# Kernel tuning notes

Hardware: AMD Instinct MI355X
Metric: run time of the kernel (lower is better)

## Reference

```python
import jax, jax.numpy as jnp
import numpy as np

N = 20000   # nodes per node type
D = 128     # hidden_dim
H = 4       # num_heads
L = 2       # num_layers
E = 80000   # edges per relation


def setup_inputs() -> dict:
    key = jax.random.key(0)
    ks = jax.random.split(key, 24)
    w = lambda i, shape: jax.random.normal(ks[i], shape, dtype=jnp.float32) * 0.05
    ei = lambda i: jax.random.randint(ks[i], (2, E), 0, N, dtype=jnp.int32)
    return {
        'x_my': jax.random.normal(ks[0], (N, D), dtype=jnp.float32),
        'x_opp': jax.random.normal(ks[1], (N, D), dtype=jnp.float32),
        'gat_beats_Wl': w(2, (L, D, H * D)),
        'gat_beats_Wr': w(3, (L, D, H * D)),
        'gat_beats_att': w(4, (L, H, D)),
        'gat_beats_b': w(5, (L, D)),
        'gat_rev_Wl': w(6, (L, D, H * D)),
        'gat_rev_Wr': w(7, (L, D, H * D)),
        'gat_rev_att': w(8, (L, H, D)),
        'gat_rev_b': w(9, (L, D)),
        'cg_lose_Wf': w(10, (L, 2 * D, D)),
        'cg_lose_bf': w(11, (L, D)),
        'cg_lose_Ws': w(12, (L, 2 * D, D)),
        'cg_lose_bs': w(13, (L, D)),
        'cg_rev_Wf': w(14, (L, 2 * D, D)),
        'cg_rev_bf': w(15, (L, D)),
        'cg_rev_Ws': w(16, (L, 2 * D, D)),
        'cg_rev_bs': w(17, (L, D)),
        'nw_W': w(18, (L, D, D)),
        'nw_b': w(19, (L, D)),
        'ei_beats': ei(20),
        'ei_loses': ei(21),
        'ei_rev_beats': ei(22),
        'ei_rev_loses': ei(23),
    }


def _segment_softmax(scores, seg, num):
    # scores [E, H]; softmax over edges sharing the same destination node
    m = jax.ops.segment_max(scores, seg, num_segments=num)
    m = jnp.where(jnp.isfinite(m), m, 0.0)  # empty segments -> -inf guard
    e = jnp.exp(scores - m[seg])
    s = jax.ops.segment_sum(e, seg, num_segments=num)
    return e / (s[seg] + 1e-16)


def _gatv2(x_src, x_dst, src, dst, Wl, Wr, att, b, num_dst):
    # PyG GATv2Conv, heads=H, concat=False, add_self_loops=False
    xl = (x_src @ Wl).reshape(x_src.shape[0], H, D)  # [Ns, H, D]
    xr = (x_dst @ Wr).reshape(x_dst.shape[0], H, D)  # [Nd, H, D]
    z = jax.nn.leaky_relu(xl[src] + xr[dst], negative_slope=0.2)  # [E, H, D]
    score = jnp.einsum('ehd,hd->eh', z, att)
    alpha = _segment_softmax(score, dst, num_dst)
    out = jax.ops.segment_sum(xl[src] * alpha[:, :, None], dst, num_segments=num_dst)
    return out.mean(axis=1) + b  # concat=False -> mean over heads, then bias


def _cgconv(x_src, x_dst, src, dst, Wf, bf, Ws, bs, num_dst):
    # PyG CGConv: z = [x_i (dst), x_j (src)], gate * softplus, aggr='add', residual
    z = jnp.concatenate([x_dst[dst], x_src[src]], axis=-1)  # [E, 2D]
    m = jax.nn.sigmoid(z @ Wf + bf) * jax.nn.softplus(z @ Ws + bs)
    return jax.ops.segment_sum(m, dst, num_segments=num_dst) + x_dst


def reference(x_my, x_opp,
              gat_beats_Wl, gat_beats_Wr, gat_beats_att, gat_beats_b,
              gat_rev_Wl, gat_rev_Wr, gat_rev_att, gat_rev_b,
              cg_lose_Wf, cg_lose_bf, cg_lose_Ws, cg_lose_bs,
              cg_rev_Wf, cg_rev_bf, cg_rev_Ws, cg_rev_bs,
              nw_W, nw_b,
              ei_beats, ei_loses, ei_rev_beats, ei_rev_loses):
    for l in range(L):
        # HeteroConv with aggr='sum': sum per-relation outputs per dst node type
        opp_new = (_gatv2(x_my, x_opp, ei_beats[0], ei_beats[1],
                          gat_beats_Wl[l], gat_beats_Wr[l], gat_beats_att[l], gat_beats_b[l],
                          x_opp.shape[0])
                   + _cgconv(x_my, x_opp, ei_loses[0], ei_loses[1],
                             cg_lose_Wf[l], cg_lose_bf[l], cg_lose_Ws[l], cg_lose_bs[l],
                             x_opp.shape[0]))
        my_new = (_cgconv(x_opp, x_my, ei_rev_beats[0], ei_rev_beats[1],
                          cg_rev_Wf[l], cg_rev_bf[l], cg_rev_Ws[l], cg_rev_bs[l],
                          x_my.shape[0])
                  + _gatv2(x_opp, x_my, ei_rev_loses[0], ei_rev_loses[1],
                           gat_rev_Wl[l], gat_rev_Wr[l], gat_rev_att[l], gat_rev_b[l],
                           x_my.shape[0]))
        # shared nodewise Linear applied to every node type
        x_my = my_new @ nw_W[l] + nw_b[l]
        x_opp = opp_new @ nw_W[l] + nw_b[l]
    return x_my, x_opp
```

## Files before the change

### kernel.cpp

```cpp
#include <hip/hip_runtime.h>
#include <hip/hip_bf16.h>
#include <cstddef>

#define NNODE 20000
#define DDIM  128
#define NHEAD 4
#define NEDGE 80000

typedef __attribute__((ext_vector_type(8))) short short8;
typedef __attribute__((ext_vector_type(4))) float f32x4;

__device__ __forceinline__ float bf2f(unsigned short u) {
  union { unsigned u32; float f; } c; c.u32 = ((unsigned)u) << 16; return c.f;
}
__device__ __forceinline__ unsigned short f2bf(float f) {
  union { float f; unsigned u; } c; c.f = f;
  unsigned u = c.u;
  unsigned r = 0x7FFFu + ((u >> 16) & 1u);
  return (unsigned short)((u + r) >> 16);
}

template<typename AT, typename OutT>
__global__ __launch_bounds__(256, 4) void gemm_mfma(
    const AT* __restrict__ A0, const unsigned short* __restrict__ B0, OutT* __restrict__ C0,
    const AT* __restrict__ A1, const unsigned short* __restrict__ B1, OutT* __restrict__ C1,
    int halfY, int M, int N, const float* __restrict__ bias)
{
  __shared__ unsigned short Bs[128 * 128];
  const int nwgx = gridDim.x;
  const int nwg = nwgx * gridDim.y;
  int orig = blockIdx.x + nwgx * blockIdx.y;
  int q8 = nwg >> 3, r8 = nwg & 7;
  int xc = orig & 7, lo = orig >> 3;
  int wg = ((xc < r8) ? xc * (q8 + 1) : r8 * (q8 + 1) + (xc - r8) * q8) + lo;
  int by = wg / nwgx;
  int bx = wg - by * nwgx;
  const AT* A = A0; const unsigned short* Bt = B0; OutT* C = C0;
  if (by >= halfY) { by -= halfY; A = A1; Bt = B1; C = C1; }
  const int bm = by * 128, bn = bx * 128;
  const int t = threadIdx.x;
  char* bsb = (char*)Bs;

  const char* btile = (const char*)(Bt + (size_t)bn * 128);
  #pragma unroll
  for (int i = 0; i < 8; ++i) {
    int fo = i * 4096 + t * 16;
    int r = fo >> 8, boff = fo & 255;
    short8 v = *reinterpret_cast<const short8*>(btile + fo);
    *reinterpret_cast<short8*>(bsb + r * 256 + (boff ^ ((r & 7) << 4))) = v;
  }
  __syncthreads();

  const int w = t >> 6, wr = w >> 1, wc = w & 1;
  const int lane = t & 63, l15 = lane & 15, lg = lane >> 4;
  const int rowl = bm + wr * 64 + l15;

  f32x4 acc[4][4];
  #pragma unroll
  for (int m = 0; m < 4; ++m)
    #pragma unroll
    for (int n = 0; n < 4; ++n) acc[m][n] = (f32x4){0.f, 0.f, 0.f, 0.f};

  #pragma unroll
  for (int kk = 0; kk < 4; ++kk) {
    const int kb = kk * 32 + lg * 8;
    short8 af[4], bfr[4];
    #pragma unroll
    for (int m = 0; m < 4; ++m) {
      if constexpr (sizeof(AT) == 4) {
        const float* ap = (const float*)A + ((size_t)(rowl + m * 16) << 7) + kb;
        float4 v0 = *reinterpret_cast<const float4*>(ap);
        float4 v1 = *reinterpret_cast<const float4*>(ap + 4);
        short8 hv;
        hv[0] = (short)f2bf(v0.x); hv[1] = (short)f2bf(v0.y);
        hv[2] = (short)f2bf(v0.z); hv[3] = (short)f2bf(v0.w);
        hv[4] = (short)f2bf(v1.x); hv[5] = (short)f2bf(v1.y);
        hv[6] = (short)f2bf(v1.z); hv[7] = (short)f2bf(v1.w);
        af[m] = hv;
      } else {
        af[m] = *reinterpret_cast<const short8*>(
            (const unsigned short*)A + ((size_t)(rowl + m * 16) << 7) + kb);
      }
    }
    const int kbyte = kb * 2;
    #pragma unroll
    for (int n = 0; n < 4; ++n) {
      int r = wc * 64 + n * 16 + l15;
      bfr[n] = *reinterpret_cast<const short8*>(bsb + r * 256 + (kbyte ^ ((r & 7) << 4)));
    }
    #pragma unroll
    for (int m = 0; m < 4; ++m)
      #pragma unroll
      for (int n = 0; n < 4; ++n)
        acc[m][n] = __builtin_amdgcn_mfma_f32_16x16x32_bf16(af[m], bfr[n], acc[m][n], 0, 0, 0);
  }

  #pragma unroll
  for (int m = 0; m < 4; ++m) {
    #pragma unroll
    for (int j = 0; j < 4; ++j) {
      int row = bm + wr * 64 + m * 16 + lg * 4 + j;
      if (row >= M) continue;
      #pragma unroll
      for (int n = 0; n < 4; ++n) {
        int col = bn + wc * 64 + n * 16 + l15;
        float v = acc[m][n][j];
        if (bias) v += bias[col];
        if constexpr (sizeof(OutT) == 2) {
          C[(size_t)row * N + col] = (OutT)f2bf(v);
        } else {
          C[(size_t)row * N + col] = v;
        }
      }
    }
  }
}

__global__ __launch_bounds__(256) void pack_gat(
    const float* __restrict__ gbWl, const float* __restrict__ gbWr,
    const float* __restrict__ grWl, const float* __restrict__ grWr,
    unsigned short* __restrict__ out)
{
  int idx = blockIdx.x * 256 + threadIdx.x;
  if (idx >= 2 * 2 * 1024 * 128) return;
  int k = idx & 127;
  int n = (idx >> 7) & 1023;
  int type = (idx >> 17) & 1;
  int l = idx >> 18;
  const float* W; int col;
  if (type == 0) { if (n < 512) { W = gbWl; col = n; } else { W = grWr; col = n - 512; } }
  else           { if (n < 512) { W = gbWr; col = n; } else { W = grWl; col = n - 512; } }
  out[idx] = f2bf(W[(size_t)l * 128 * 512 + (size_t)k * 512 + col]);
}

__global__ __launch_bounds__(256) void pack_cg(
    const float* __restrict__ clWf, const float* __restrict__ clWs,
    const float* __restrict__ crWf, const float* __restrict__ crWs,
    unsigned short* __restrict__ out)
{
  int idx = blockIdx.x * 256 + threadIdx.x;
  if (idx >= 2 * 2 * 512 * 128) return;
  int k = idx & 127;
  int n = (idx >> 7) & 511;
  int type = (idx >> 16) & 1;
  int l = idx >> 17;
  int blk = n >> 7, c = n & 127;
  const float* W; int row;
  if (type == 0) {
    if (blk == 0) { W = clWf; row = 128 + k; }
    else if (blk == 1) { W = clWs; row = 128 + k; }
    else if (blk == 2) { W = crWf; row = k; }
    else { W = crWs; row = k; }
  } else {
    if (blk == 0) { W = clWf; row = k; }
    else if (blk == 1) { W = clWs; row = k; }
    else if (blk == 2) { W = crWf; row = 128 + k; }
    else { W = crWs; row = 128 + k; }
  }
  out[idx] = f2bf(W[(size_t)l * 256 * 128 + (size_t)row * 128 + c]);
}

__global__ __launch_bounds__(256) void pack_nw(
    const float* __restrict__ nwW, unsigned short* __restrict__ out)
{
  int idx = blockIdx.x * 256 + threadIdx.x;
  if (idx >= 2 * 128 * 128) return;
  int k = idx & 127;
  int n = (idx >> 7) & 127;
  int l = idx >> 14;
  out[idx] = f2bf(nwW[(size_t)l * 128 * 128 + (size_t)k * 128 + n]);
}

__global__ __launch_bounds__(256) void f2b_kernel(
    const float* __restrict__ in, unsigned short* __restrict__ out, int n)
{
  int idx = (blockIdx.x * 256 + threadIdx.x) * 8;
  if (idx >= n) return;
  float4 a = *reinterpret_cast<const float4*>(in + idx);
  float4 b = *reinterpret_cast<const float4*>(in + idx + 4);
  short8 o;
  o[0] = (short)f2bf(a.x); o[1] = (short)f2bf(a.y);
  o[2] = (short)f2bf(a.z); o[3] = (short)f2bf(a.w);
  o[4] = (short)f2bf(b.x); o[5] = (short)f2bf(b.y);
  o[6] = (short)f2bf(b.z); o[7] = (short)f2bf(b.w);
  *reinterpret_cast<short8*>(out + idx) = o;
}

__global__ __launch_bounds__(256) void build_buckets(
    const int* __restrict__ e0, const int* __restrict__ e1,
    const int* __restrict__ e2, const int* __restrict__ e3,
    unsigned* __restrict__ cnt, int* __restrict__ bucket)
{
  int idx = blockIdx.x * 256 + threadIdx.x;
  if (idx >= 4 * NEDGE) return;
  int set = idx / NEDGE;
  int e = idx - set * NEDGE;
  const int* ei = (set == 0) ? e0 : (set == 1) ? e1 : (set == 2) ? e2 : e3;
  int s = ei[e], d = ei[NEDGE + e];
  unsigned slot = atomicAdd(&cnt[set * NNODE + d], 1u);
  if (slot < 64u) bucket[((size_t)set * NNODE + d) * 64 + slot] = s;
}

__global__ __launch_bounds__(256) void edge_fused(
    const unsigned short* __restrict__ xlA, const unsigned short* __restrict__ xrA,
    const unsigned short* __restrict__ FsA, const unsigned short* __restrict__ SsA,
    const unsigned short* __restrict__ FdA, const unsigned short* __restrict__ SdA,
    const unsigned short* __restrict__ xresA,
    const int* __restrict__ bgA, const unsigned* __restrict__ cgA,
    const int* __restrict__ bcA, const unsigned* __restrict__ ccA,
    const float* __restrict__ attA, const float* __restrict__ biasA,
    const float* __restrict__ bfA, const float* __restrict__ bsA,
    float* __restrict__ accA,
    const unsigned short* __restrict__ xlB, const unsigned short* __restrict__ xrB,
    const unsigned short* __restrict__ FsB, const unsigned short* __restrict__ SsB,
    const unsigned short* __restrict__ FdB, const unsigned short* __restrict__ SdB,
    const unsigned short* __restrict__ xresB,
    const int* __restrict__ bgB, const unsigned* __restrict__ cgB,
    const int* __restrict__ bcB, const unsigned* __restrict__ ccB,
    const float* __restrict__ attB, const float* __restrict__ biasB,
    const float* __restrict__ bfB, const float* __restrict__ bsB,
    float* __restrict__ accB, int nwb)
{
  int blk = blockIdx.x;
  int second = (blk >= nwb) ? 1 : 0;
  if (second) blk -= nwb;
  int d = blk * 4 + (threadIdx.x >> 6);
  int lane = threadIdx.x & 63;
  int h = lane >> 4, q = lane & 15;

  const unsigned short* xl  = second ? xlB  : xlA;
  const unsigned short* xr  = second ? xrB  : xrA;
  const unsigned short* Fs  = second ? FsB  : FsA;
  const unsigned short* Ss  = second ? SsB  : SsA;
  const unsigned short* Fd  = second ? FdB  : FdA;
  const unsigned short* Sd  = second ? SdB  : SdA;
  const unsigned short* xres = second ? xresB : xresA;
  const int* bg = second ? bgB : bgA;
  const unsigned* cg = second ? cgB : cgA;
  const int* bc = second ? bcB : bcA;
  const unsigned* cc = second ? ccB : ccA;
  const float* att  = second ? attB  : attA;
  const float* bias = second ? biasB : biasA;
  const float* bf_  = second ? bfB   : bfA;
  const float* bs_  = second ? bsB   : bsA;
  float* acc = second ? accB : accA;

  unsigned ng = cg[d]; ng = (ng > 64u) ? 64u : ng;
  short8 xrv = *reinterpret_cast<const short8*>(xr + (size_t)d * 1024 + h * 128 + q * 8);
  float4 at0 = *reinterpret_cast<const float4*>(att + h * 128 + q * 8);
  float4 at1 = *reinterpret_cast<const float4*>(att + h * 128 + q * 8 + 4);
  float xrf[8], atf[8];
  atf[0] = at0.x; atf[1] = at0.y; atf[2] = at0.z; atf[3] = at0.w;
  atf[4] = at1.x; atf[5] = at1.y; atf[6] = at1.z; atf[7] = at1.w;
  #pragma unroll
  for (int j = 0; j < 8; ++j) xrf[j] = bf2f((unsigned short)xrv[j]);

  float uout[8] = {0.f, 0.f, 0.f, 0.f, 0.f, 0.f, 0.f, 0.f};
  float ssum = 0.f;
  const int* bkg = bg + (size_t)d * 64;
  short8 xln = {0,0,0,0,0,0,0,0};
  if (ng > 0) {
    int s0 = bkg[0];
    xln = *reinterpret_cast<const short8*>(xl + (size_t)s0 * 1024 + h * 128 + q * 8);
  }
  for (unsigned i = 0; i < ng; ++i) {
    short8 xlv = xln;
    if (i + 1 < ng) {
      int s2 = bkg[i + 1];
      xln = *reinterpret_cast<const short8*>(xl + (size_t)s2 * 1024 + h * 128 + q * 8);
    }
    float xlf[8];
    #pragma unroll
    for (int j = 0; j < 8; ++j) xlf[j] = bf2f((unsigned short)xlv[j]);
    float sum = 0.f;
    #pragma unroll
    for (int j = 0; j < 8; ++j) {
      float z = xlf[j] + xrf[j];
      z = (z > 0.f) ? z : 0.2f * z;
      sum += atf[j] * z;
    }
    #pragma unroll
    for (int m = 1; m < 16; m <<= 1) sum += __shfl_xor(sum, m);
    float e = __expf(fminf(sum, 80.f));
    ssum += e;
    #pragma unroll
    for (int j = 0; j < 8; ++j) uout[j] += e * xlf[j];
  }
  float scale = __builtin_amdgcn_rcpf(ssum + 1e-16f) * 0.25f;
  #pragma unroll
  for (int j = 0; j < 8; ++j) {
    float v = uout[j] * scale;
    v += __shfl_xor(v, 16);
    v += __shfl_xor(v, 32);
    uout[j] = v;
  }

  unsigned nc = cc[d]; nc = (nc > 64u) ? 64u : nc;
  float fd[8], sd[8], ac[8];
  {
    short8 fdv = *reinterpret_cast<const short8*>(Fd + (size_t)d * 512 + q * 8);
    short8 sdv = *reinterpret_cast<const short8*>(Sd + (size_t)d * 512 + q * 8);
    const float* bfp = bf_ + q * 8;
    const float* bsp = bs_ + q * 8;
    #pragma unroll
    for (int j = 0; j < 8; ++j) {
      fd[j] = bf2f((unsigned short)fdv[j]) + bfp[j];
      sd[j] = bf2f((unsigned short)sdv[j]) + bsp[j];
      ac[j] = 0.f;
    }
  }
  const int* bkc = bc + (size_t)d * 64;
  short8 fsn = {0,0,0,0,0,0,0,0}, ssn = {0,0,0,0,0,0,0,0};
  unsigned i0 = (unsigned)h;
  if (i0 < nc) {
    int s0 = bkc[i0];
    fsn = *reinterpret_cast<const short8*>(Fs + (size_t)s0 * 512 + q * 8);
    ssn = *reinterpret_cast<const short8*>(Ss + (size_t)s0 * 512 + q * 8);
  }
  for (unsigned i = i0; i < nc; i += 4) {
    short8 fsv = fsn, ssv = ssn;
    if (i + 4 < nc) {
      int s2 = bkc[i + 4];
      fsn = *reinterpret_cast<const short8*>(Fs + (size_t)s2 * 512 + q * 8);
      ssn = *reinterpret_cast<const short8*>(Ss + (size_t)s2 * 512 + q * 8);
    }
    #pragma unroll
    for (int j = 0; j < 8; ++j) {
      float g  = fd[j] + bf2f((unsigned short)fsv[j]);
      float tt = sd[j] + bf2f((unsigned short)ssv[j]);
      float gate = __builtin_amdgcn_rcpf(1.f + __expf(-g));
      float sp = fmaxf(tt, 0.f) + __logf(1.f + __expf(-fabsf(tt)));
      ac[j] += gate * sp;
    }
  }
  #pragma unroll
  for (int j = 0; j < 8; ++j) {
    float v = ac[j];
    v += __shfl_xor(v, 16);
    v += __shfl_xor(v, 32);
    ac[j] = v;
  }

  if (h == 0) {
    short8 xs = *reinterpret_cast<const short8*>(xres + (size_t)d * 128 + q * 8);
    const float* bp = bias + q * 8;
    float4 o0, o1;
    o0.x = uout[0] + ac[0] + bf2f((unsigned short)xs[0]) + bp[0];
    o0.y = uout[1] + ac[1] + bf2f((unsigned short)xs[1]) + bp[1];
    o0.z = uout[2] + ac[2] + bf2f((unsigned short)xs[2]) + bp[2];
    o0.w = uout[3] + ac[3] + bf2f((unsigned short)xs[3]) + bp[3];
    o1.x = uout[4] + ac[4] + bf2f((unsigned short)xs[4]) + bp[4];
    o1.y = uout[5] + ac[5] + bf2f((unsigned short)xs[5]) + bp[5];
    o1.z = uout[6] + ac[6] + bf2f((unsigned short)xs[6]) + bp[6];
    o1.w = uout[7] + ac[7] + bf2f((unsigned short)xs[7]) + bp[7];
    *reinterpret_cast<float4*>(acc + (size_t)d * 128 + q * 8) = o0;
    *reinterpret_cast<float4*>(acc + (size_t)d * 128 + q * 8 + 4) = o1;
  }
}


extern "C" void kernel_launch(void* const* d_in, const int* in_sizes, int n_in,
                              void* d_out, int out_size, void* d_ws, size_t ws_size,
                              hipStream_t stream) {
  const float* x_my_in  = (const float*)d_in[0];
  const float* x_opp_in = (const float*)d_in[1];
  const float* gb_Wl  = (const float*)d_in[2];
  const float* gb_Wr  = (const float*)d_in[3];
  const float* gb_att = (const float*)d_in[4];
  const float* gb_b   = (const float*)d_in[5];
  const float* gr_Wl  = (const float*)d_in[6];
  const float* gr_Wr  = (const float*)d_in[7];
  const float* gr_att = (const float*)d_in[8];
  const float* gr_b   = (const float*)d_in[9];
  const float* cl_Wf  = (const float*)d_in[10];
  const float* cl_bf  = (const float*)d_in[11];
  const float* cl_Ws  = (const float*)d_in[12];
  const float* cl_bs  = (const float*)d_in[13];
  const float* cr_Wf  = (const float*)d_in[14];
  const float* cr_bf  = (const float*)d_in[15];
  const float* cr_Ws  = (const float*)d_in[16];
  const float* cr_bs  = (const float*)d_in[17];
  const float* nw_W   = (const float*)d_in[18];
  const float* nw_b   = (const float*)d_in[19];
  const int* ei_beats     = (const int*)d_in[20];
  const int* ei_loses     = (const int*)d_in[21];
  const int* ei_rev_beats = (const int*)d_in[22];
  const int* ei_rev_loses = (const int*)d_in[23];

  float* out = (float*)d_out;

  const size_t ND = (size_t)NNODE * DDIM;
  unsigned short* XAb = (unsigned short*)d_ws;
  float* NM  = (float*)(XAb + 2 * ND);
  float* NO  = NM + ND;
  unsigned short* PJM = (unsigned short*)(NM + 2 * ND);
  unsigned short* PJO = PJM + (size_t)NNODE * 1024;
  unsigned short* PCM = PJO + (size_t)NNODE * 1024;
  unsigned short* PCO = PCM + (size_t)NNODE * 512;
  unsigned* CNT = (unsigned*)(PCO + (size_t)NNODE * 512);
  int* BKT = (int*)(CNT + 4 * NNODE);
  unsigned short* PKG = (unsigned short*)(BKT + (size_t)4 * NNODE * 64);
  unsigned short* PKC = PKG + 2 * 2 * 1024 * 128;
  unsigned short* PKN = PKC + 2 * 2 * 512 * 128;

  const int cvb = (int)(ND / 8 + 255) / 256;
  const int nwb = NNODE / 4;

  hipLaunchKernelGGL(pack_gat, dim3(2 * 2 * 1024 * 128 / 256), dim3(256), 0, stream,
                     gb_Wl, gb_Wr, gr_Wl, gr_Wr, PKG);
  hipLaunchKernelGGL(pack_cg, dim3(2 * 2 * 512 * 128 / 256), dim3(256), 0, stream,
                     cl_Wf, cl_Ws, cr_Wf, cr_Ws, PKC);
  hipLaunchKernelGGL(pack_nw, dim3(2 * 128 * 128 / 256), dim3(256), 0, stream, nw_W, PKN);

  hipLaunchKernelGGL(f2b_kernel, dim3(cvb), dim3(256), 0, stream, x_my_in,  XAb,      (int)ND);
  hipLaunchKernelGGL(f2b_kernel, dim3(cvb), dim3(256), 0, stream, x_opp_in, XAb + ND, (int)ND);

  hipMemsetAsync(CNT, 0, 4 * NNODE * sizeof(unsigned), stream);
  hipLaunchKernelGGL(build_buckets, dim3((4 * NEDGE + 255) / 256), dim3(256), 0, stream,
                     ei_beats, ei_rev_loses, ei_loses, ei_rev_beats, CNT, BKT);

  for (int l = 0; l < 2; ++l) {
    const size_t oA = (size_t)l * NHEAD * DDIM;
    const size_t oB = (size_t)l * DDIM;

    hipLaunchKernelGGL((gemm_mfma<unsigned short, unsigned short>), dim3(8, 314), dim3(256), 0, stream,
                       XAb,      PKG + (size_t)(l * 2 + 0) * 1024 * 128, PJM,
                       XAb + ND, PKG + (size_t)(l * 2 + 1) * 1024 * 128, PJO,
                       157, NNODE, 1024, (const float*)nullptr);

    hipLaunchKernelGGL((gemm_mfma<unsigned short, unsigned short>), dim3(4, 314), dim3(256), 0, stream,
                       XAb,      PKC + (size_t)(l * 2 + 0) * 512 * 128, PCM,
                       XAb + ND, PKC + (size_t)(l * 2 + 1) * 512 * 128, PCO,
                       157, NNODE, 512, (const float*)nullptr);

    hipLaunchKernelGGL(edge_fused, dim3(2 * nwb), dim3(256), 0, stream,
                        PJM, PJO,
                        PCM, PCM + 128, PCO, PCO + 128,
                        XAb + ND,
                       BKT + (size_t)0 * NNODE * 64, CNT + 0 * NNODE,
                       BKT + (size_t)2 * NNODE * 64, CNT + 2 * NNODE,
                       gb_att + oA, gb_b + oB, cl_bf + oB, cl_bs + oB, NO,
                        PJO + 512, PJM + 512,
                        PCO + 256, PCO + 384, PCM + 256, PCM + 384,
                        XAb,
                       BKT + (size_t)1 * NNODE * 64, CNT + 1 * NNODE,
                       BKT + (size_t)3 * NNODE * 64, CNT + 3 * NNODE,
                       gr_att + oA, gr_b + oB, cr_bf + oB, cr_bs + oB, NM,
                       nwb);

    if (l == 0) {
      hipLaunchKernelGGL((gemm_mfma<float, unsigned short>), dim3(1, 313), dim3(256), 0, stream,
                         NM, PKN + (size_t)l * 128 * 128, XAb,
                         NM, PKN + (size_t)l * 128 * 128, XAb,
                         313, 2 * NNODE, 128, nw_b + oB);
    } else {
      hipLaunchKernelGGL((gemm_mfma<float, float>), dim3(1, 313), dim3(256), 0, stream,
                         NM, PKN + (size_t)l * 128 * 128, out,
                         NM, PKN + (size_t)l * 128 * 128, out,
                         313, 2 * NNODE, 128, nw_b + oB);
    }
  }
  (void)in_sizes; (void)n_in; (void)out_size; (void)ws_size;
}
```

Measured before the change: 439.8 us.

## Merge GAT and CGConv projection GEMMs into one wide GEMM and batch gathers

Packs the GAT and CGConv weights into one 1536-column matrix per layer, so a single GEMM per layer produces both projections into an interleaved row-strided buffer. Also merges the weight-pack and float-to-bf16 conversion kernels into single launches. In the edge kernel, the first four GAT source rows and the first two CGConv rows per lane are loaded up front instead of one-ahead prefetching, to raise memory-level parallelism. The cost is a wider stride in the gathered rows, which may spread them across more cache lines, plus higher register pressure.

```diff
diff --git a/kernel.cpp b/kernel.cpp
--- a/kernel.cpp
+++ b/kernel.cpp
@@ -6,6 +6,7 @@
 #define DDIM  128
 #define NHEAD 4
 #define NEDGE 80000
+#define PSTR  1536
 
 typedef __attribute__((ext_vector_type(8))) short short8;
 typedef __attribute__((ext_vector_type(4))) float f32x4;
@@ -116,68 +117,64 @@
   }
 }
 
-__global__ __launch_bounds__(256) void pack_gat(
+__global__ __launch_bounds__(256) void pack_all(
     const float* __restrict__ gbWl, const float* __restrict__ gbWr,
     const float* __restrict__ grWl, const float* __restrict__ grWr,
-    unsigned short* __restrict__ out)
+    const float* __restrict__ clWf, const float* __restrict__ clWs,
+    const float* __restrict__ crWf, const float* __restrict__ crWs,
+    const float* __restrict__ nwW,
+    unsigned short* __restrict__ PKU, unsigned short* __restrict__ PKN)
 {
   int idx = blockIdx.x * 256 + threadIdx.x;
-  if (idx >= 2 * 2 * 1024 * 128) return;
-  int k = idx & 127;
-  int n = (idx >> 7) & 1023;
-  int type = (idx >> 17) & 1;
-  int l = idx >> 18;
-  const float* W; int col;
-  if (type == 0) { if (n < 512) { W = gbWl; col = n; } else { W = grWr; col = n - 512; } }
-  else           { if (n < 512) { W = gbWr; col = n; } else { W = grWl; col = n - 512; } }
-  out[idx] = f2bf(W[(size_t)l * 128 * 512 + (size_t)k * 512 + col]);
-}
-
-__global__ __launch_bounds__(256) void pack_cg(
-    const float* __restrict__ clWf, const float* __restrict__ clWs,
-    const float* __restrict__ crWf, const float* __restrict__ crWs,
-    unsigned short* __restrict__ out)
-{
-  int idx = blockIdx.x * 256 + threadIdx.x;
-  if (idx >= 2 * 2 * 512 * 128) return;
-  int k = idx & 127;
-  int n = (idx >> 7) & 511;
-  int type = (idx >> 16) & 1;
-  int l = idx >> 17;
-  int blk = n >> 7, c = n & 127;
-  const float* W; int row;
-  if (type == 0) {
-    if (blk == 0) { W = clWf; row = 128 + k; }
-    else if (blk == 1) { W = clWs; row = 128 + k; }
-    else if (blk == 2) { W = crWf; row = k; }
-    else { W = crWs; row = k; }
-  } else {
-    if (blk == 0) { W = clWf; row = k; }
-    else if (blk == 1) { W = clWs; row = k; }
-    else if (blk == 2) { W = crWf; row = 128 + k; }
-    else { W = crWs; row = 128 + k; }
-  }
-  out[idx] = f2bf(W[(size_t)l * 256 * 128 + (size_t)row * 128 + c]);
-}
-
-__global__ __launch_bounds__(256) void pack_nw(
-    const float* __restrict__ nwW, unsigned short* __restrict__ out)
-{
-  int idx = blockIdx.x * 256 + threadIdx.x;
-  if (idx >= 2 * 128 * 128) return;
-  int k = idx & 127;
-  int n = (idx >> 7) & 127;
-  int l = idx >> 14;
-  out[idx] = f2bf(nwW[(size_t)l * 128 * 128 + (size_t)k * 128 + n]);
-}
-
-__global__ __launch_bounds__(256) void f2b_kernel(
-    const float* __restrict__ in, unsigned short* __restrict__ out, int n)
+  const int NU = 2 * 2 * PSTR * 128;
+  if (idx < NU) {
+    int k = idx & 127;
+    int r = idx >> 7;
+    int n = r % PSTR;
+    int rt = r / PSTR;
+    int type = rt & 1, l = rt >> 1;
+    float v;
+    if (n < 1024) {
+      const float* W; int col;
+      if (type == 0) { if (n < 512) { W = gbWl; col = n; } else { W = grWr; col = n - 512; } }
+      else           { if (n < 512) { W = gbWr; col = n; } else { W = grWl; col = n - 512; } }
+      v = W[(size_t)l * 128 * 512 + (size_t)k * 512 + col];
+    } else {
+      int nn = n - 1024, blk = nn >> 7, c = nn & 127;
+      const float* W; int row;
+      if (type == 0) {
+        if (blk == 0) { W = clWf; row = 128 + k; }
+        else if (blk == 1) { W = clWs; row = 128 + k; }
+        else if (blk == 2) { W = crWf; row = k; }
+        else { W = crWs; row = k; }
+      } else {
+        if (blk == 0) { W = clWf; row = k; }
+        else if (blk == 1) { W = clWs; row = k; }
+        else if (blk == 2) { W = crWf; row = 128 + k; }
+        else { W = crWs; row = 128 + k; }
+      }
+      v = W[(size_t)l * 256 * 128 + (size_t)row * 128 + c];
+    }
+    PKU[idx] = f2bf(v);
+    return;
+  }
+  int i2 = idx - NU;
+  if (i2 >= 2 * 128 * 128) return;
+  int k = i2 & 127;
+  int n = (i2 >> 7) & 127;
+  int l = i2 >> 14;
+  PKN[i2] = f2bf(nwW[(size_t)l * 128 * 128 + (size_t)k * 128 + n]);
+}
+
+__global__ __launch_bounds__(256) void f2b_all(
+    const float* __restrict__ inA, const float* __restrict__ inB,
+    unsigned short* __restrict__ out, int nhalf)
 {
   int idx = (blockIdx.x * 256 + threadIdx.x) * 8;
-  if (idx >= n) return;
-  float4 a = *reinterpret_cast<const float4*>(in + idx);
-  float4 b = *reinterpret_cast<const float4*>(in + idx + 4);
+  if (idx >= 2 * nhalf) return;
+  const float* src = (idx < nhalf) ? inA + idx : inB + (idx - nhalf);
+  float4 a = *reinterpret_cast<const float4*>(src);
+  float4 b = *reinterpret_cast<const float4*>(src + 4);
   short8 o;
   o[0] = (short)f2bf(a.x); o[1] = (short)f2bf(a.y);
   o[2] = (short)f2bf(a.z); o[3] = (short)f2bf(a.w);
@@ -202,51 +199,49 @@
 }
 
 __global__ __launch_bounds__(256) void edge_fused(
-    const unsigned short* __restrict__ xlA, const unsigned short* __restrict__ xrA,
-    const unsigned short* __restrict__ FsA, const unsigned short* __restrict__ SsA,
-    const unsigned short* __restrict__ FdA, const unsigned short* __restrict__ SdA,
-    const unsigned short* __restrict__ xresA,
-    const int* __restrict__ bgA, const unsigned* __restrict__ cgA,
-    const int* __restrict__ bcA, const unsigned* __restrict__ ccA,
-    const float* __restrict__ attA, const float* __restrict__ biasA,
-    const float* __restrict__ bfA, const float* __restrict__ bsA,
-    float* __restrict__ accA,
-    const unsigned short* __restrict__ xlB, const unsigned short* __restrict__ xrB,
-    const unsigned short* __restrict__ FsB, const unsigned short* __restrict__ SsB,
-    const unsigned short* __restrict__ FdB, const unsigned short* __restrict__ SdB,
-    const unsigned short* __restrict__ xresB,
-    const int* __restrict__ bgB, const unsigned* __restrict__ cgB,
-    const int* __restrict__ bcB, const unsigned* __restrict__ ccB,
-    const float* __restrict__ attB, const float* __restrict__ biasB,
-    const float* __restrict__ bfB, const float* __restrict__ bsB,
-    float* __restrict__ accB, int nwb)
+    const unsigned short* __restrict__ PJM_, const unsigned short* __restrict__ PJO_,
+    const unsigned short* __restrict__ XAb_,
+    const int* __restrict__ BKT_, const unsigned* __restrict__ CNT_,
+    const float* __restrict__ gb_att, const float* __restrict__ gb_b,
+    const float* __restrict__ cl_bf, const float* __restrict__ cl_bs,
+    const float* __restrict__ gr_att, const float* __restrict__ gr_b,
+    const float* __restrict__ cr_bf, const float* __restrict__ cr_bs,
+    float* __restrict__ NM_, float* __restrict__ NO_, int nwb)
 {
   int blk = blockIdx.x;
-  int second = (blk >= nwb) ? 1 : 0;
+  int second = blk >= nwb;
   if (second) blk -= nwb;
   int d = blk * 4 + (threadIdx.x >> 6);
   int lane = threadIdx.x & 63;
   int h = lane >> 4, q = lane & 15;
 
-  const unsigned short* xl  = second ? xlB  : xlA;
-  const unsigned short* xr  = second ? xrB  : xrA;
-  const unsigned short* Fs  = second ? FsB  : FsA;
-  const unsigned short* Ss  = second ? SsB  : SsA;
-  const unsigned short* Fd  = second ? FdB  : FdA;
-  const unsigned short* Sd  = second ? SdB  : SdA;
-  const unsigned short* xres = second ? xresB : xresA;
-  const int* bg = second ? bgB : bgA;
-  const unsigned* cg = second ? cgB : cgA;
-  const int* bc = second ? bcB : bcA;
-  const unsigned* cc = second ? ccB : ccA;
-  const float* att  = second ? attB  : attA;
-  const float* bias = second ? biasB : biasA;
-  const float* bf_  = second ? bfB   : bfA;
-  const float* bs_  = second ? bsB   : bsA;
-  float* acc = second ? accB : accA;
+  const unsigned short *xl, *xr, *Fs, *Ss, *Fd, *Sd, *xres;
+  const int *bg, *bc;
+  const unsigned *cg, *cc;
+  const float *att, *bias, *bf_, *bs_;
+  float* acc;
+  if (!second) {
+    xl = PJM_;        xr = PJO_;
+    Fs = PJM_ + 1024; Ss = PJM_ + 1152;
+    Fd = PJO_ + 1024; Sd = PJO_ + 1152;
+    xres = XAb_ + (size_t)NNODE * DDIM;
+    bg = BKT_;                              cg = CNT_;
+    bc = BKT_ + (size_t)2 * NNODE * 64;     cc = CNT_ + 2 * NNODE;
+    att = gb_att; bias = gb_b; bf_ = cl_bf; bs_ = cl_bs; acc = NO_;
+  } else {
+    xl = PJO_ + 512;  xr = PJM_ + 512;
+    Fs = PJO_ + 1280; Ss = PJO_ + 1408;
+    Fd = PJM_ + 1280; Sd = PJM_ + 1408;
+    xres = XAb_;
+    bg = BKT_ + (size_t)1 * NNODE * 64;     cg = CNT_ + 1 * NNODE;
+    bc = BKT_ + (size_t)3 * NNODE * 64;     cc = CNT_ + 3 * NNODE;
+    att = gr_att; bias = gr_b; bf_ = cr_bf; bs_ = cr_bs; acc = NM_;
+  }
 
   unsigned ng = cg[d]; ng = (ng > 64u) ? 64u : ng;
-  short8 xrv = *reinterpret_cast<const short8*>(xr + (size_t)d * 1024 + h * 128 + q * 8);
+  const int* bkg = bg + (size_t)d * 64;
+  const size_t off = (size_t)h * 128 + q * 8;
+  short8 xrv = *reinterpret_cast<const short8*>(xr + (size_t)d * PSTR + off);
   float4 at0 = *reinterpret_cast<const float4*>(att + h * 128 + q * 8);
   float4 at1 = *reinterpret_cast<const float4*>(att + h * 128 + q * 8 + 4);
   float xrf[8], atf[8];
@@ -257,34 +252,38 @@
 
   float uout[8] = {0.f, 0.f, 0.f, 0.f, 0.f, 0.f, 0.f, 0.f};
   float ssum = 0.f;
-  const int* bkg = bg + (size_t)d * 64;
-  short8 xln = {0,0,0,0,0,0,0,0};
+
+#define GATP(XLV) { \
+    float xlf[8]; \
+    _Pragma("unroll") for (int j = 0; j < 8; ++j) xlf[j] = bf2f((unsigned short)(XLV)[j]); \
+    float sum = 0.f; \
+    _Pragma("unroll") for (int j = 0; j < 8; ++j) { \
+      float z = xlf[j] + xrf[j]; \
+      z = (z > 0.f) ? z : 0.2f * z; \
+      sum += atf[j] * z; } \
+    _Pragma("unroll") for (int m = 1; m < 16; m <<= 1) sum += __shfl_xor(sum, m); \
+    float e = __expf(fminf(sum, 80.f)); \
+    ssum += e; \
+    _Pragma("unroll") for (int j = 0; j < 8; ++j) uout[j] += e * xlf[j]; }
+
   if (ng > 0) {
     int s0 = bkg[0];
-    xln = *reinterpret_cast<const short8*>(xl + (size_t)s0 * 1024 + h * 128 + q * 8);
-  }
-  for (unsigned i = 0; i < ng; ++i) {
-    short8 xlv = xln;
-    if (i + 1 < ng) {
-      int s2 = bkg[i + 1];
-      xln = *reinterpret_cast<const short8*>(xl + (size_t)s2 * 1024 + h * 128 + q * 8);
-    }
-    float xlf[8];
-    #pragma unroll
-    for (int j = 0; j < 8; ++j) xlf[j] = bf2f((unsigned short)xlv[j]);
-    float sum = 0.f;
-    #pragma unroll
-    for (int j = 0; j < 8; ++j) {
-      float z = xlf[j] + xrf[j];
-      z = (z > 0.f) ? z : 0.2f * z;
-      sum += atf[j] * z;
-    }
-    #pragma unroll
-    for (int m = 1; m < 16; m <<= 1) sum += __shfl_xor(sum, m);
-    float e = __expf(fminf(sum, 80.f));
-    ssum += e;
-    #pragma unroll
-    for (int j = 0; j < 8; ++j) uout[j] += e * xlf[j];
+    int s1 = bkg[(ng > 1u) ? 1 : 0];
+    int s2 = bkg[(ng > 2u) ? 2 : 0];
+    int s3 = bkg[(ng > 3u) ? 3 : 0];
+    short8 x0 = *reinterpret_cast<const short8*>(xl + (size_t)s0 * PSTR + off);
+    short8 x1 = *reinterpret_cast<const short8*>(xl + (size_t)s1 * PSTR + off);
+    short8 x2 = *reinterpret_cast<const short8*>(xl + (size_t)s2 * PSTR + off);
+    short8 x3 = *reinterpret_cast<const short8*>(xl + (size_t)s3 * PSTR + off);
+    GATP(x0);
+    if (ng > 1u) GATP(x1);
+    if (ng > 2u) GATP(x2);
+    if (ng > 3u) GATP(x3);
+    for (unsigned i = 4; i < ng; ++i) {
+      int s = bkg[i];
+      short8 xv = *reinterpret_cast<const short8*>(xl + (size_t)s * PSTR + off);
+      GATP(xv);
+    }
   }
   float scale = __builtin_amdgcn_rcpf(ssum + 1e-16f) * 0.25f;
   #pragma unroll
@@ -296,10 +295,12 @@
   }
 
   unsigned nc = cc[d]; nc = (nc > 64u) ? 64u : nc;
+  const int* bkc = bc + (size_t)d * 64;
+  const size_t offc = (size_t)q * 8;
   float fd[8], sd[8], ac[8];
   {
-    short8 fdv = *reinterpret_cast<const short8*>(Fd + (size_t)d * 512 + q * 8);
-    short8 sdv = *reinterpret_cast<const short8*>(Sd + (size_t)d * 512 + q * 8);
+    short8 fdv = *reinterpret_cast<const short8*>(Fd + (size_t)d * PSTR + offc);
+    short8 sdv = *reinterpret_cast<const short8*>(Sd + (size_t)d * PSTR + offc);
     const float* bfp = bf_ + q * 8;
     const float* bsp = bs_ + q * 8;
     #pragma unroll
@@ -309,28 +310,33 @@
       ac[j] = 0.f;
     }
   }
-  const int* bkc = bc + (size_t)d * 64;
-  short8 fsn = {0,0,0,0,0,0,0,0}, ssn = {0,0,0,0,0,0,0,0};
-  unsigned i0 = (unsigned)h;
-  if (i0 < nc) {
-    int s0 = bkc[i0];
-    fsn = *reinterpret_cast<const short8*>(Fs + (size_t)s0 * 512 + q * 8);
-    ssn = *reinterpret_cast<const short8*>(Ss + (size_t)s0 * 512 + q * 8);
-  }
-  for (unsigned i = i0; i < nc; i += 4) {
-    short8 fsv = fsn, ssv = ssn;
-    if (i + 4 < nc) {
-      int s2 = bkc[i + 4];
-      fsn = *reinterpret_cast<const short8*>(Fs + (size_t)s2 * 512 + q * 8);
-      ssn = *reinterpret_cast<const short8*>(Ss + (size_t)s2 * 512 + q * 8);
-    }
-    #pragma unroll
-    for (int j = 0; j < 8; ++j) {
-      float g  = fd[j] + bf2f((unsigned short)fsv[j]);
-      float tt = sd[j] + bf2f((unsigned short)ssv[j]);
-      float gate = __builtin_amdgcn_rcpf(1.f + __expf(-g));
-      float sp = fmaxf(tt, 0.f) + __logf(1.f + __expf(-fabsf(tt)));
-      ac[j] += gate * sp;
+
+#define CGP(FV, SV) { \
+    _Pragma("unroll") for (int j = 0; j < 8; ++j) { \
+      float g  = fd[j] + bf2f((unsigned short)(FV)[j]); \
+      float tt = sd[j] + bf2f((unsigned short)(SV)[j]); \
+      float gate = __builtin_amdgcn_rcpf(1.f + __expf(-g)); \
+      float sp = fmaxf(tt, 0.f) + __logf(1.f + __expf(-fabsf(tt))); \
+      ac[j] += gate * sp; } }
+
+  {
+    unsigned ia = (unsigned)h, ib2 = (unsigned)h + 4u;
+    bool pa = ia < nc, pb = ib2 < nc;
+    int sa = pa ? bkc[ia] : 0;
+    int sb = pb ? bkc[ib2] : 0;
+    short8 fa = {0,0,0,0,0,0,0,0}, sav = {0,0,0,0,0,0,0,0};
+    short8 fb = {0,0,0,0,0,0,0,0}, sbv = {0,0,0,0,0,0,0,0};
+    if (pa) { fa  = *reinterpret_cast<const short8*>(Fs + (size_t)sa * PSTR + offc);
+              sav = *reinterpret_cast<const short8*>(Ss + (size_t)sa * PSTR + offc); }
+    if (pb) { fb  = *reinterpret_cast<const short8*>(Fs + (size_t)sb * PSTR + offc);
+              sbv = *reinterpret_cast<const short8*>(Ss + (size_t)sb * PSTR + offc); }
+    if (pa) CGP(fa, sav);
+    if (pb) CGP(fb, sbv);
+    for (unsigned i = (unsigned)h + 8u; i < nc; i += 4u) {
+      int s = bkc[i];
+      short8 fv = *reinterpret_cast<const short8*>(Fs + (size_t)s * PSTR + offc);
+      short8 sv = *reinterpret_cast<const short8*>(Ss + (size_t)s * PSTR + offc);
+      CGP(fv, sv);
     }
   }
   #pragma unroll
@@ -394,26 +400,20 @@
   float* NM  = (float*)(XAb + 2 * ND);
   float* NO  = NM + ND;
   unsigned short* PJM = (unsigned short*)(NM + 2 * ND);
-  unsigned short* PJO = PJM + (size_t)NNODE * 1024;
-  unsigned short* PCM = PJO + (size_t)NNODE * 1024;
-  unsigned short* PCO = PCM + (size_t)NNODE * 512;
-  unsigned* CNT = (unsigned*)(PCO + (size_t)NNODE * 512);
+  unsigned short* PJO = PJM + (size_t)NNODE * PSTR;
+  unsigned* CNT = (unsigned*)(PJO + (size_t)NNODE * PSTR);
   int* BKT = (int*)(CNT + 4 * NNODE);
-  unsigned short* PKG = (unsigned short*)(BKT + (size_t)4 * NNODE * 64);
-  unsigned short* PKC = PKG + 2 * 2 * 1024 * 128;
-  unsigned short* PKN = PKC + 2 * 2 * 512 * 128;
-
-  const int cvb = (int)(ND / 8 + 255) / 256;
+  unsigned short* PKU = (unsigned short*)(BKT + (size_t)4 * NNODE * 64);
+  unsigned short* PKN = PKU + 2 * 2 * PSTR * 128;
+
   const int nwb = NNODE / 4;
 
-  hipLaunchKernelGGL(pack_gat, dim3(2 * 2 * 1024 * 128 / 256), dim3(256), 0, stream,
-                     gb_Wl, gb_Wr, gr_Wl, gr_Wr, PKG);
-  hipLaunchKernelGGL(pack_cg, dim3(2 * 2 * 512 * 128 / 256), dim3(256), 0, stream,
-                     cl_Wf, cl_Ws, cr_Wf, cr_Ws, PKC);
-  hipLaunchKernelGGL(pack_nw, dim3(2 * 128 * 128 / 256), dim3(256), 0, stream, nw_W, PKN);
-
-  hipLaunchKernelGGL(f2b_kernel, dim3(cvb), dim3(256), 0, stream, x_my_in,  XAb,      (int)ND);
-  hipLaunchKernelGGL(f2b_kernel, dim3(cvb), dim3(256), 0, stream, x_opp_in, XAb + ND, (int)ND);
+  hipLaunchKernelGGL(pack_all, dim3((2 * 2 * PSTR * 128 + 2 * 128 * 128) / 256), dim3(256),
+                     0, stream, gb_Wl, gb_Wr, gr_Wl, gr_Wr,
+                     cl_Wf, cl_Ws, cr_Wf, cr_Ws, nw_W, PKU, PKN);
+
+  hipLaunchKernelGGL(f2b_all, dim3((int)(2 * ND / 8 / 256)), dim3(256), 0, stream,
+                     x_my_in, x_opp_in, XAb, (int)ND);
 
   hipMemsetAsync(CNT, 0, 4 * NNODE * sizeof(unsigned), stream);
   hipLaunchKernelGGL(build_buckets, dim3((4 * NEDGE + 255) / 256), dim3(256), 0, stream,
@@ -423,30 +423,16 @@
     const size_t oA = (size_t)l * NHEAD * DDIM;
     const size_t oB = (size_t)l * DDIM;
 
-    hipLaunchKernelGGL((gemm_mfma<unsigned short, unsigned short>), dim3(8, 314), dim3(256), 0, stream,
-                       XAb,      PKG + (size_t)(l * 2 + 0) * 1024 * 128, PJM,
-                       XAb + ND, PKG + (size_t)(l * 2 + 1) * 1024 * 128, PJO,
-                       157, NNODE, 1024, (const float*)nullptr);
-
-    hipLaunchKernelGGL((gemm_mfma<unsigned short, unsigned short>), dim3(4, 314), dim3(256), 0, stream,
-                       XAb,      PKC + (size_t)(l * 2 + 0) * 512 * 128, PCM,
-                       XAb + ND, PKC + (size_t)(l * 2 + 1) * 512 * 128, PCO,
-                       157, NNODE, 512, (const float*)nullptr);
+    hipLaunchKernelGGL((gemm_mfma<unsigned short, unsigned short>), dim3(12, 314), dim3(256), 0, stream,
+                       XAb,      PKU + (size_t)(l * 2 + 0) * PSTR * 128, PJM,
+                       XAb + ND, PKU + (size_t)(l * 2 + 1) * PSTR * 128, PJO,
+                       157, NNODE, PSTR, (const float*)nullptr);
 
     hipLaunchKernelGGL(edge_fused, dim3(2 * nwb), dim3(256), 0, stream,
-                        PJM, PJO,
-                        PCM, PCM + 128, PCO, PCO + 128,
-                        XAb + ND,
-                       BKT + (size_t)0 * NNODE * 64, CNT + 0 * NNODE,
-                       BKT + (size_t)2 * NNODE * 64, CNT + 2 * NNODE,
-                       gb_att + oA, gb_b + oB, cl_bf + oB, cl_bs + oB, NO,
-                        PJO + 512, PJM + 512,
-                        PCO + 256, PCO + 384, PCM + 256, PCM + 384,
-                        XAb,
-                       BKT + (size_t)1 * NNODE * 64, CNT + 1 * NNODE,
-                       BKT + (size_t)3 * NNODE * 64, CNT + 3 * NNODE,
-                       gr_att + oA, gr_b + oB, cr_bf + oB, cr_bs + oB, NM,
-                       nwb);
+                       PJM, PJO, XAb, BKT, CNT,
+                       gb_att + oA, gb_b + oB, cl_bf + oB, cl_bs + oB,
+                       gr_att + oA, gr_b + oB, cr_bf + oB, cr_bs + oB,
+                       NM, NO, nwb);
 
     if (l == 0) {
       hipLaunchKernelGGL((gemm_mfma<float, unsigned short>), dim3(1, 313), dim3(256), 0, stream,
```

Measured after the change: 437.4 us. Within noise of the previous version (-0.5%).
